# Kernel optimization log

Hardware: AMD Instinct MI355X
Metric: run time of the kernel (lower is better)

Reference implementation:

```python
import jax, jax.numpy as jnp
import numpy as np

B, T, F, H, O = 64, 500, 89, 512, 72


def setup_inputs() -> dict:
    key = jax.random.key(0)
    ks = jax.random.split(key, 16)
    d = {
        "batch": jax.random.normal(ks[0], (B, T, F), dtype=jnp.float32),
        "lengths": jax.random.randint(ks[1], (B,), 250, T + 1),
    }
    in_sizes = [F, 2 * H, 2 * H]  # layer 0 takes features, layers 1-2 take bidir output
    for i, fi in enumerate(in_sizes):
        d[f"w{i}"] = jax.random.normal(ks[2 + 3 * i], (2 * H, fi), dtype=jnp.float32) / np.sqrt(fi).astype(np.float32)
        d[f"b{i}"] = jnp.zeros((2 * H,), jnp.float32)
        d[f"u{i}"] = jax.random.normal(ks[3 + 3 * i], (2 * H, H), dtype=jnp.float32) / np.sqrt(H).astype(np.float32)
    d["wfc"] = jax.random.normal(ks[12], (O, 2 * H), dtype=jnp.float32) / np.sqrt(2 * H).astype(np.float32)
    d["bfc"] = jnp.zeros((O,), jnp.float32)
    return d


def _ligru_bidir(x, W, b, U):
    # SpeechBrain LiGRU layer: fwd and bwd directions share weights; the
    # time-flipped copy is stacked along the batch dim and one scan is run.
    Bx = x.shape[0]
    xb = jnp.concatenate([x, x[:, ::-1]], axis=0)            # [2B, T, in]
    gates_x = jnp.einsum('btf,gf->tbg', xb, W) + b           # [T, 2B, 2H] precomputed input gates
    h0 = jnp.zeros((2 * Bx, H), x.dtype)

    def step(h, g):
        g = g + h @ U.T                                       # [2B, 2H]
        at, zt = jnp.split(g, 2, axis=-1)
        zt = jax.nn.sigmoid(zt)
        h = zt * h + (1.0 - zt) * jnp.tanh(at)                # nonlinearity='tanh'
        return h, h

    _, hs = jax.lax.scan(step, h0, gates_x)                   # [T, 2B, H]
    hs = jnp.swapaxes(hs, 0, 1)                               # [2B, T, H]
    return jnp.concatenate([hs[:Bx], hs[Bx:, ::-1]], axis=2)  # [B, T, 2H]


def reference(batch, lengths, w0, b0, u0, w1, b1, u1, w2, b2, u2, wfc, bfc):
    x = batch
    for W, b, U in ((w0, b0, u0), (w1, b1, u1), (w2, b2, u2)):
        x = _ligru_bidir(x, W, b, U)
    out = jnp.einsum('bth,oh->bto', x, wfc) + bfc             # [B, T, O]
    # Pack valid frames per utterance: predictions[p:p+len_i] = out[i, :len_i]
    mask = (jnp.arange(T)[None, :] < lengths[:, None]).ravel()  # [B*T]
    order = jnp.argsort(jnp.logical_not(mask), stable=True)     # valid rows first, in order
    total = int(np.asarray(lengths).sum())
    return out.reshape(B * T, O)[order][:total]
```

## Files before the change

kernel.cpp:

```cpp
#include <hip/hip_runtime.h>

typedef _Float16 f16;
typedef _Float16 half8 __attribute__((ext_vector_type(8)));
typedef float f32x4 __attribute__((ext_vector_type(4)));
typedef unsigned int u32;
typedef u32 u32x2 __attribute__((ext_vector_type(2)));
typedef u32 u32x4 __attribute__((ext_vector_type(4)));

__device__ inline float frcp(float x) {
#if __has_builtin(__builtin_amdgcn_rcpf)
  return __builtin_amdgcn_rcpf(x);
#else
  return 1.0f / x;
#endif
}
__device__ inline float fexp2(float x) {
#if __has_builtin(__builtin_amdgcn_exp2f)
  return __builtin_amdgcn_exp2f(x);
#else
  return exp2f(x);
#endif
}


__global__ void k_cvt(const float* __restrict__ s, f16* __restrict__ d, int n) {
  int i = blockIdx.x * 256 + threadIdx.x;
  if (i < n) d[i] = (f16)s[i];
}

__global__ void k_zero(u32* __restrict__ p, int n) {
  int i = blockIdx.x * 256 + threadIdx.x;
  if (i < n) p[i] = 0u;
}

__global__ void k_w0pad(const float* __restrict__ w0, f16* __restrict__ d) {
  int i = blockIdx.x * 256 + threadIdx.x;
  if (i >= 1024 * 96) return;
  int row = i / 96, c = i % 96;
  d[i] = (c < 89) ? (f16)w0[row * 89 + c] : (f16)0.f;
}

__global__ void k_xb0(const float* __restrict__ x, f16* __restrict__ d) {
  int i = blockIdx.x * 256 + threadIdx.x;
  if (i >= 128 * 500 * 96) return;
  int f = i % 96;
  int t = (i / 96) % 500;
  int s = i / (96 * 500);
  float v = 0.f;
  if (f < 89) {
    if (s < 64) v = x[((size_t)s * 500 + t) * 89 + f];
    else        v = x[((size_t)(s - 64) * 500 + (499 - t)) * 89 + f];
  }
  d[i] = (f16)v;
}

__global__ void k_offs(const int* __restrict__ lens, int* __restrict__ offs) {
  if (threadIdx.x == 0 && blockIdx.x == 0) {
    int s = 0;
    for (int i = 0; i < 64; ++i) { offs[i] = s; s += lens[i]; }
  }
}

template <int MODE>
__global__ __launch_bounds__(256) void k_gates(const f16* __restrict__ Aw,
                                               const f16* __restrict__ W16,
                                               const float* __restrict__ bias,
                                               f16* __restrict__ gates) {
  constexpr int KW = MODE ? 1024 : 96;
  const int t = blockIdx.x;
  const int nb = blockIdx.y * 128;
  const int tid = threadIdx.x;
  const int w = tid >> 6, l = tid & 63, c = l & 15, rg = l >> 4;
  const int wr = w >> 1, wc = w & 1;

  __shared__ f16 As[128 * 32];
  __shared__ f16 Bs[128 * 32];

  f32x4 acc[4][4] = {};

  const int srow = tid >> 1;
  const int seg = (tid & 1) * 16;
  const int ch0 = seg >> 3;
  const int wsw = (srow >> 1) & 3;

  for (int kb = 0; kb < KW; kb += 32) {
    const f16* pa;
    if (MODE == 0) {
      pa = Aw + ((size_t)srow * 500 + t) * 96 + kb + seg;
    } else {
      int f0 = kb + seg;
      int half = f0 >> 9;
      int col = f0 & 511;
      int s = srow;
      int seq, time;
      if (s < 64) { seq = half ? 64 + s : s;  time = half ? 499 - t : t; }
      else        { seq = half ? s : s - 64;  time = half ? t : 499 - t; }
      pa = Aw + ((size_t)seq * 500 + time) * 512 + col;
    }
    const f16* pb = W16 + (size_t)(nb + srow) * KW + kb + seg;
    half8 a0 = *(const half8*)pa;
    half8 a1 = *(const half8*)(pa + 8);
    half8 b0 = *(const half8*)pb;
    half8 b1 = *(const half8*)(pb + 8);
    __syncthreads();
    *(half8*)&As[srow * 32 + ((ch0 + 0) ^ wsw) * 8] = a0;
    *(half8*)&As[srow * 32 + ((ch0 + 1) ^ wsw) * 8] = a1;
    *(half8*)&Bs[srow * 32 + ((ch0 + 0) ^ wsw) * 8] = b0;
    *(half8*)&Bs[srow * 32 + ((ch0 + 1) ^ wsw) * 8] = b1;
    __syncthreads();
    half8 aF[4], bF[4];
#pragma unroll
    for (int i = 0; i < 4; ++i) {
      int row = wr * 64 + i * 16 + c;
      aF[i] = *(const half8*)&As[row * 32 + ((rg ^ ((row >> 1) & 3)) * 8)];
    }
#pragma unroll
    for (int j = 0; j < 4; ++j) {
      int row = wc * 64 + j * 16 + c;
      bF[j] = *(const half8*)&Bs[row * 32 + ((rg ^ ((row >> 1) & 3)) * 8)];
    }
#pragma unroll
    for (int i = 0; i < 4; ++i)
#pragma unroll
      for (int j = 0; j < 4; ++j)
        acc[i][j] = __builtin_amdgcn_mfma_f32_16x16x32_f16(aF[i], bF[j], acc[i][j], 0, 0, 0);
  }

#pragma unroll
  for (int j = 0; j < 4; ++j) {
    int n = nb + wc * 64 + j * 16 + c;
    float bj = bias[n];
#pragma unroll
    for (int i = 0; i < 4; ++i) {
#pragma unroll
      for (int r = 0; r < 4; ++r) {
        int m = wr * 64 + i * 16 + rg * 4 + r;
        gates[((size_t)t * 128 + m) * 1024 + n] = (f16)(acc[i][j][r] + bj);
      }
    }
  }
}

__global__ __launch_bounds__(256, 1) void k_rec(const f16* __restrict__ gates,
                                                const f16* __restrict__ U,
                                                f16* __restrict__ hs,
                                                f16* __restrict__ hx,
                                                u32* __restrict__ flags,
                                                int tagbase) {
  const int sg = blockIdx.x & 7, cg = blockIdx.x >> 3;
  const int tid = threadIdx.x;
  const int l = tid & 63, w = tid >> 6, c = l & 15, rg = l >> 4;
  const int s0 = sg * 16;
  const int hcol = cg * 64 + w * 16;
  const int an0 = hcol, zn0 = 512 + hcol;

  __shared__ f16 hlds[8192 + 4 * 256];

  half8 ua[16], uz[16];
#pragma unroll
  for (int kt = 0; kt < 16; ++kt) {
    ua[kt] = *(const half8*)(U + (size_t)(an0 + c) * 512 + kt * 32 + rg * 8);
    uz[kt] = *(const half8*)(U + (size_t)(zn0 + c) * 512 + kt * 32 + rg * 8);
  }

  float hold[4] = {0.f, 0.f, 0.f, 0.f};

  f16 ga[4], gz[4];
  {
    const f16* gb = gates + ((size_t)0 * 128 + s0 + rg * 4) * 1024;
#pragma unroll
    for (int r = 0; r < 4; ++r) { ga[r] = gb[r * 1024 + an0 + c]; gz[r] = gb[r * 1024 + zn0 + c]; }
  }

  const int ktp = cg * 2 + (w >> 1);
  const int pbase = ktp * 512 + (w & 1) * 256;
  f16* scr = &hlds[8192 + w * 256];
  const int scri = (c >> 3) * 128 + (c & 7);
  const int srow2 = (l >> 1) & 15;
  const int col2 = ktp * 32 + ((w & 1) * 2 + (l >> 5)) * 8 + (l & 1) * 4;

  const size_t tileoff = (size_t)sg * 8192;

  for (int t = 0; t < 500; ++t) {
#pragma unroll
    for (int kt = 0; kt < 16; ++kt) asm volatile("" : "+v"(ua[kt]), "+v"(uz[kt]));

    u32x4 d0, d1, d2, d3;
    if (t == 0) {
      d0 = (u32x4){0u, 0u, 0u, 0u}; d1 = d0; d2 = d0; d3 = d0;
    } else {
      const u32 tgt = (u32)(tagbase + t);
      const u32* fl = flags + sg * 32 + (l & 31);
      int guard = 0;
      for (;;) {
        u32 f = __hip_atomic_load(fl, __ATOMIC_RELAXED, __HIP_MEMORY_SCOPE_AGENT);
        if (__all((int)(f >= tgt))) break;
        if (++guard > (1 << 15)) break;
      }
      const f16* src = hx + (size_t)(t & 1) * 65536 + tileoff + (size_t)tid * 32;
      asm volatile("global_load_dwordx4 %0, %1, off sc0 sc1" : "=v"(d0) : "v"(src) : "memory");
      asm volatile("global_load_dwordx4 %0, %1, off sc0 sc1" : "=v"(d1) : "v"(src + 8) : "memory");
      asm volatile("global_load_dwordx4 %0, %1, off sc0 sc1" : "=v"(d2) : "v"(src + 16) : "memory");
      asm volatile("global_load_dwordx4 %0, %1, off sc0 sc1" : "=v"(d3) : "v"(src + 24) : "memory");
      asm volatile("s_waitcnt vmcnt(0)"
                   : "+v"(d0), "+v"(d1), "+v"(d2), "+v"(d3) : : "memory");
    }
    *(u32x4*)&hlds[tid * 32 + 0]  = d0;
    *(u32x4*)&hlds[tid * 32 + 8]  = d1;
    *(u32x4*)&hlds[tid * 32 + 16] = d2;
    *(u32x4*)&hlds[tid * 32 + 24] = d3;
    __syncthreads();

    f32x4 acc_a, acc_z;
#pragma unroll
    for (int r = 0; r < 4; ++r) { acc_a[r] = (float)ga[r]; acc_z[r] = (float)gz[r]; }
#pragma unroll
    for (int kt = 0; kt < 16; ++kt) {
      half8 aF = *(const half8*)&hlds[kt * 512 + l * 8];
      acc_a = __builtin_amdgcn_mfma_f32_16x16x32_f16(aF, ua[kt], acc_a, 0, 0, 0);
      acc_z = __builtin_amdgcn_mfma_f32_16x16x32_f16(aF, uz[kt], acc_z, 0, 0, 0);
    }

#pragma unroll
    for (int r = 0; r < 4; ++r) {
      float av = acc_a[r];
      float zv = acc_z[r];
      float zs = frcp(1.f + fexp2(-1.44269504f * zv));
      float u2 = fexp2(2.88539008f * av);
      float th = 1.f - 2.f * frcp(u2 + 1.f);
      float hn = th + zs * (hold[r] - th);
      hold[r] = hn;
      scr[scri + (rg * 4 + r) * 8] = (f16)hn;
    }
    u32x2 pkt = *(const u32x2*)&scr[l * 4];
    {
      f16* dst = hx + (size_t)((t + 1) & 1) * 65536 + tileoff + pbase + (size_t)l * 4;
      asm volatile("global_store_dwordx2 %0, %1, off sc0 sc1" :: "v"(dst), "v"(pkt) : "memory");
    }
    asm volatile("s_waitcnt vmcnt(0)" ::: "memory");
    if (l == 0)
      __hip_atomic_store(&flags[sg * 32 + cg * 4 + w], (u32)(tagbase + t + 1),
                         __ATOMIC_RELAXED, __HIP_MEMORY_SCOPE_AGENT);

    *(u32x2*)&hs[((size_t)(s0 + srow2) * 500 + t) * 512 + col2] = pkt;

    int tn = (t + 1 < 500) ? t + 1 : 499;
    const f16* gb = gates + ((size_t)tn * 128 + s0 + rg * 4) * 1024;
#pragma unroll
    for (int r = 0; r < 4; ++r) { ga[r] = gb[r * 1024 + an0 + c]; gz[r] = gb[r * 1024 + zn0 + c]; }
  }
}

__global__ __launch_bounds__(256) void k_fc(const f16* __restrict__ hs,
                                            const f16* __restrict__ wfc,
                                            const float* __restrict__ bfc,
                                            const int* __restrict__ lens,
                                            const int* __restrict__ offs,
                                            float* __restrict__ out) {
  const int b = blockIdx.x, chunk = blockIdx.y;
  const int tid = threadIdx.x;
  __shared__ f16 X[16][1032];
#pragma unroll
  for (int ii = 0; ii < 8; ++ii) {
    int sg = ii * 256 + tid;
    int row = sg >> 7;
    int f = (sg & 127) * 8;
    int t = chunk * 16 + row;
    int tt = t < 500 ? t : 499;
    int half = f >> 9, col = f & 511;
    int seq = half ? 64 + b : b;
    int time = half ? 499 - tt : tt;
    *(half8*)&X[row][f] = *(const half8*)&hs[((size_t)seq * 500 + time) * 512 + col];
  }
  __syncthreads();
  int row = tid >> 4, og = tid & 15;
  int t = chunk * 16 + row;
  int len = lens[b];
  float acc[5];
#pragma unroll
  for (int j = 0; j < 5; ++j) {
    int o = j * 16 + og;
    acc[j] = (o < 72) ? bfc[o] : 0.f;
  }
  for (int k8 = 0; k8 < 128; ++k8) {
    half8 x8 = *(const half8*)&X[row][k8 * 8];
    float xf[8];
#pragma unroll
    for (int e = 0; e < 8; ++e) xf[e] = (float)x8[e];
#pragma unroll
    for (int j = 0; j < 5; ++j) {
      int o = j * 16 + og;
      int oc = o < 72 ? o : 0;
      half8 w8 = *(const half8*)&wfc[(size_t)oc * 1024 + k8 * 8];
#pragma unroll
      for (int e = 0; e < 8; ++e) acc[j] += xf[e] * (float)w8[e];
    }
  }
  if (t < 500 && t < len) {
    size_t base = ((size_t)offs[b] + t) * 72;
#pragma unroll
    for (int j = 0; j < 5; ++j) {
      int o = j * 16 + og;
      if (o < 72) out[base + o] = acc[j];
    }
  }
}


extern "C" void kernel_launch(void* const* d_in, const int* in_sizes, int n_in,
                              void* d_out, int out_size, void* d_ws, size_t ws_size,
                              hipStream_t stream) {
  const float* batch = (const float*)d_in[0];
  const int*   lens  = (const int*)d_in[1];
  const float* w0 = (const float*)d_in[2];
  const float* b0 = (const float*)d_in[3];
  const float* u0 = (const float*)d_in[4];
  const float* w1 = (const float*)d_in[5];
  const float* b1 = (const float*)d_in[6];
  const float* u1 = (const float*)d_in[7];
  const float* w2 = (const float*)d_in[8];
  const float* b2 = (const float*)d_in[9];
  const float* u2 = (const float*)d_in[10];
  const float* wfc = (const float*)d_in[11];
  const float* bfc = (const float*)d_in[12];
  float* out = (float*)d_out;

  char* ws = (char*)d_ws;
  const size_t GATES_OFF = 0;
  const size_t HS_OFF    = 131072000;
  const size_t XB0_OFF   = 196608000;
  const size_t W0P_OFF   = 208896000;
  const size_t W1_OFF    = 209092608;
  const size_t W2_OFF    = 211189760;
  const size_t U0_OFF    = 213286912;
  const size_t U1_OFF    = 214335488;
  const size_t U2_OFF    = 215384064;
  const size_t WFC_OFF   = 216432640;
  const size_t OFFS_OFF  = 216580096;
  const size_t HX_OFF    = 216581120;
  const size_t FLAGS_OFF = 216843264;

  f16* g_gates = (f16*)(ws + GATES_OFF);
  f16* g_hs    = (f16*)(ws + HS_OFF);
  f16* g_xb0   = (f16*)(ws + XB0_OFF);
  f16* g_w0p   = (f16*)(ws + W0P_OFF);
  f16* g_w1    = (f16*)(ws + W1_OFF);
  f16* g_w2    = (f16*)(ws + W2_OFF);
  f16* g_u0    = (f16*)(ws + U0_OFF);
  f16* g_u1    = (f16*)(ws + U1_OFF);
  f16* g_u2    = (f16*)(ws + U2_OFF);
  f16* g_wfc   = (f16*)(ws + WFC_OFF);
  int* g_offs  = (int*)(ws + OFFS_OFF);
  f16* g_hx    = (f16*)(ws + HX_OFF);
  u32* g_flags = (u32*)(ws + FLAGS_OFF);

  hipLaunchKernelGGL(k_offs, dim3(1), dim3(64), 0, stream, lens, g_offs);

  auto cvt = [&](const float* s, f16* d, int n) {
    hipLaunchKernelGGL(k_cvt, dim3((n + 255) / 256), dim3(256), 0, stream, s, d, n);
  };
  cvt(w1, g_w1, 1024 * 1024);
  cvt(w2, g_w2, 1024 * 1024);
  cvt(u0, g_u0, 1024 * 512);
  cvt(u1, g_u1, 1024 * 512);
  cvt(u2, g_u2, 1024 * 512);
  cvt(wfc, g_wfc, 72 * 1024);
  hipLaunchKernelGGL(k_w0pad, dim3((1024 * 96 + 255) / 256), dim3(256), 0, stream, w0, g_w0p);
  hipLaunchKernelGGL(k_xb0, dim3((128 * 500 * 96 + 255) / 256), dim3(256), 0, stream, batch, g_xb0);
  hipLaunchKernelGGL(k_zero, dim3(1), dim3(256), 0, stream, g_flags, 256);

  hipLaunchKernelGGL((k_gates<0>), dim3(500, 8), dim3(256), 0, stream, g_xb0, g_w0p, b0, g_gates);
  hipLaunchKernelGGL(k_rec, dim3(64), dim3(256), 0, stream, g_gates, g_u0, g_hs, g_hx, g_flags, 0);
  hipLaunchKernelGGL((k_gates<1>), dim3(500, 8), dim3(256), 0, stream, g_hs, g_w1, b1, g_gates);
  hipLaunchKernelGGL(k_rec, dim3(64), dim3(256), 0, stream, g_gates, g_u1, g_hs, g_hx, g_flags, 512);
  hipLaunchKernelGGL((k_gates<1>), dim3(500, 8), dim3(256), 0, stream, g_hs, g_w2, b2, g_gates);
  hipLaunchKernelGGL(k_rec, dim3(64), dim3(256), 0, stream, g_gates, g_u2, g_hs, g_hx, g_flags, 1024);

  hipLaunchKernelGGL(k_fc, dim3(64, 32), dim3(256), 0, stream, g_hs, g_wfc, bfc, lens, g_offs, out);
}
```

Baseline: 4.898 ms.

## Stage recurrent weights in LDS and prefetch fragment-ordered gates four steps ahead

Measured after the change: 6.323 ms. 29.1% more time.

```diff
diff --git a/kernel.cpp b/kernel.cpp
--- a/kernel.cpp
+++ b/kernel.cpp
@@ -126,16 +126,23 @@
         acc[i][j] = __builtin_amdgcn_mfma_f32_16x16x32_f16(aF[i], bF[j], acc[i][j], 0, 0, 0);
   }
 
+  const int tq = t >> 2, ts = t & 3;
 #pragma unroll
   for (int j = 0; j < 4; ++j) {
     int n = nb + wc * 64 + j * 16 + c;
     float bj = bias[n];
+    int az = n >> 9, nn = n & 511;
+    int cg2 = nn >> 6, w2 = (nn >> 4) & 3, c2 = nn & 15;
 #pragma unroll
     for (int i = 0; i < 4; ++i) {
 #pragma unroll
       for (int r = 0; r < 4; ++r) {
         int m = wr * 64 + i * 16 + rg * 4 + r;
-        gates[((size_t)t * 128 + m) * 1024 + n] = (f16)(acc[i][j][r] + bj);
+        int sg2 = m >> 4, sr = m & 15;
+        int l2 = (sr >> 2) * 16 + c2;
+        size_t off = (size_t)tq * 524288 + (size_t)sg2 * 65536 + (size_t)cg2 * 8192 +
+                     (size_t)w2 * 2048 + (size_t)l2 * 32 + ts * 8 + az * 4 + (sr & 3);
+        gates[off] = (f16)(acc[i][j][r] + bj);
       }
     }
   }
@@ -147,107 +154,128 @@
                                                 f16* __restrict__ hx,
                                                 u32* __restrict__ flags,
                                                 int tagbase) {
-  const int sg = blockIdx.x & 7, cg = blockIdx.x >> 3;
+  extern __shared__ f16 smem[];
+  f16* ulds = smem;
+  f16* hlds = smem + 65536;
+  f16* scrb = smem + 65536 + 8192;
+
+  const int bid = blockIdx.x;
+  const int sg = bid & 7, cg = bid >> 3;
   const int tid = threadIdx.x;
   const int l = tid & 63, w = tid >> 6, c = l & 15, rg = l >> 4;
   const int s0 = sg * 16;
-  const int hcol = cg * 64 + w * 16;
-  const int an0 = hcol, zn0 = 512 + hcol;
-
-  __shared__ f16 hlds[8192 + 4 * 256];
-
-  half8 ua[16], uz[16];
-#pragma unroll
-  for (int kt = 0; kt < 16; ++kt) {
-    ua[kt] = *(const half8*)(U + (size_t)(an0 + c) * 512 + kt * 32 + rg * 8);
-    uz[kt] = *(const half8*)(U + (size_t)(zn0 + c) * 512 + kt * 32 + rg * 8);
-  }
-
-  float hold[4] = {0.f, 0.f, 0.f, 0.f};
-
-  f16 ga[4], gz[4];
+
   {
-    const f16* gb = gates + ((size_t)0 * 128 + s0 + rg * 4) * 1024;
-#pragma unroll
-    for (int r = 0; r < 4; ++r) { ga[r] = gb[r * 1024 + an0 + c]; gz[r] = gb[r * 1024 + zn0 + c]; }
-  }
+    const f16* Ua = U + (size_t)cg * 64 * 512;
+    const f16* Uz = U + (size_t)(512 + cg * 64) * 512;
+#pragma unroll
+    for (int it = 0; it < 16; ++it) {
+      int rr = (it & 3) * 16 + c;
+      int chunk = (it >> 2) * 16 + w * 4 + rg;
+      int col = chunk * 8;
+      half8 va = *(const half8*)(Ua + (size_t)rr * 512 + col);
+      half8 vz = *(const half8*)(Uz + (size_t)rr * 512 + col);
+      int wv = rr >> 4, cc = rr & 15, kt = col >> 5, rg2 = (col >> 3) & 3;
+      int base = (wv * 32 + kt) * 512 + (rg2 * 16 + cc) * 8;
+      *(half8*)&ulds[base] = va;
+      *(half8*)&ulds[base + 8192] = vz;
+    }
+  }
+  __syncthreads();
 
   const int ktp = cg * 2 + (w >> 1);
   const int pbase = ktp * 512 + (w & 1) * 256;
-  f16* scr = &hlds[8192 + w * 256];
-  const int scri = (c >> 3) * 128 + (c & 7);
+  f16* scr = scrb + w * 384;
   const int srow2 = (l >> 1) & 15;
   const int col2 = ktp * 32 + ((w & 1) * 2 + (l >> 5)) * 8 + (l & 1) * 4;
-
   const size_t tileoff = (size_t)sg * 8192;
-
-  for (int t = 0; t < 500; ++t) {
-#pragma unroll
-    for (int kt = 0; kt < 16; ++kt) asm volatile("" : "+v"(ua[kt]), "+v"(uz[kt]));
-
-    u32x4 d0, d1, d2, d3;
-    if (t == 0) {
-      d0 = (u32x4){0u, 0u, 0u, 0u}; d1 = d0; d2 = d0; d3 = d0;
-    } else {
-      const u32 tgt = (u32)(tagbase + t);
-      const u32* fl = flags + sg * 32 + (l & 31);
-      int guard = 0;
-      for (;;) {
-        u32 f = __hip_atomic_load(fl, __ATOMIC_RELAXED, __HIP_MEMORY_SCOPE_AGENT);
-        if (__all((int)(f >= tgt))) break;
-        if (++guard > (1 << 15)) break;
+  const u32* flbase = flags + sg * 32;
+  u32* myflag = flags + sg * 32 + cg * 4 + w;
+
+  const f16* gbase = gates + (size_t)sg * 65536 + (size_t)cg * 8192 +
+                     (size_t)w * 2048 + (size_t)l * 32;
+  u32x4 gcur[4], gnxt[4];
+#pragma unroll
+  for (int q = 0; q < 4; ++q) gcur[q] = *(const u32x4*)(gbase + q * 8);
+
+  float hold[4] = {0.f, 0.f, 0.f, 0.f};
+
+  for (int tb = 0; tb < 125; ++tb) {
+#pragma unroll
+    for (int ts = 0; ts < 4; ++ts) {
+      const int t = tb * 4 + ts;
+      u32x4 d0, d1, d2, d3;
+      if (t == 0) {
+        d0 = (u32x4){0u, 0u, 0u, 0u}; d1 = d0; d2 = d0; d3 = d0;
+      } else {
+        const u32 tgt = (u32)(tagbase + t);
+        const u32* fl = flbase + (l & 31);
+        int g2 = 0;
+        for (;;) {
+          u32 f = __hip_atomic_load(fl, __ATOMIC_RELAXED, __HIP_MEMORY_SCOPE_AGENT);
+          if (__all((int)(f >= tgt))) break;
+          if (++g2 > (1 << 15)) break;
+        }
+        const f16* src = hx + (size_t)(t & 1) * 65536 + tileoff + (size_t)tid * 32;
+        asm volatile("global_load_dwordx4 %0, %1, off sc0 sc1" : "=v"(d0) : "v"(src) : "memory");
+        asm volatile("global_load_dwordx4 %0, %1, off sc0 sc1" : "=v"(d1) : "v"(src + 8) : "memory");
+        asm volatile("global_load_dwordx4 %0, %1, off sc0 sc1" : "=v"(d2) : "v"(src + 16) : "memory");
+        asm volatile("global_load_dwordx4 %0, %1, off sc0 sc1" : "=v"(d3) : "v"(src + 24) : "memory");
+        asm volatile("s_waitcnt vmcnt(0)"
+                     : "+v"(d0), "+v"(d1), "+v"(d2), "+v"(d3) : : "memory");
       }
-      const f16* src = hx + (size_t)(t & 1) * 65536 + tileoff + (size_t)tid * 32;
-      asm volatile("global_load_dwordx4 %0, %1, off sc0 sc1" : "=v"(d0) : "v"(src) : "memory");
-      asm volatile("global_load_dwordx4 %0, %1, off sc0 sc1" : "=v"(d1) : "v"(src + 8) : "memory");
-      asm volatile("global_load_dwordx4 %0, %1, off sc0 sc1" : "=v"(d2) : "v"(src + 16) : "memory");
-      asm volatile("global_load_dwordx4 %0, %1, off sc0 sc1" : "=v"(d3) : "v"(src + 24) : "memory");
-      asm volatile("s_waitcnt vmcnt(0)"
-                   : "+v"(d0), "+v"(d1), "+v"(d2), "+v"(d3) : : "memory");
-    }
-    *(u32x4*)&hlds[tid * 32 + 0]  = d0;
-    *(u32x4*)&hlds[tid * 32 + 8]  = d1;
-    *(u32x4*)&hlds[tid * 32 + 16] = d2;
-    *(u32x4*)&hlds[tid * 32 + 24] = d3;
-    __syncthreads();
-
-    f32x4 acc_a, acc_z;
-#pragma unroll
-    for (int r = 0; r < 4; ++r) { acc_a[r] = (float)ga[r]; acc_z[r] = (float)gz[r]; }
-#pragma unroll
-    for (int kt = 0; kt < 16; ++kt) {
-      half8 aF = *(const half8*)&hlds[kt * 512 + l * 8];
-      acc_a = __builtin_amdgcn_mfma_f32_16x16x32_f16(aF, ua[kt], acc_a, 0, 0, 0);
-      acc_z = __builtin_amdgcn_mfma_f32_16x16x32_f16(aF, uz[kt], acc_z, 0, 0, 0);
-    }
-
-#pragma unroll
-    for (int r = 0; r < 4; ++r) {
-      float av = acc_a[r];
-      float zv = acc_z[r];
-      float zs = frcp(1.f + fexp2(-1.44269504f * zv));
-      float u2 = fexp2(2.88539008f * av);
-      float th = 1.f - 2.f * frcp(u2 + 1.f);
-      float hn = th + zs * (hold[r] - th);
-      hold[r] = hn;
-      scr[scri + (rg * 4 + r) * 8] = (f16)hn;
-    }
-    u32x2 pkt = *(const u32x2*)&scr[l * 4];
-    {
+
+      if (ts == 0) {
+        int tqn = (tb < 124) ? tb + 1 : 124;
+        const f16* gb2 = gbase + (size_t)tqn * 524288;
+#pragma unroll
+        for (int q = 0; q < 4; ++q) gnxt[q] = *(const u32x4*)(gb2 + q * 8);
+      }
+
+      *(u32x4*)&hlds[tid * 32 + 0]  = d0;
+      *(u32x4*)&hlds[tid * 32 + 8]  = d1;
+      *(u32x4*)&hlds[tid * 32 + 16] = d2;
+      *(u32x4*)&hlds[tid * 32 + 24] = d3;
+      __syncthreads();
+
+      f32x4 acc_a, acc_z;
+      const half8 gv = __builtin_bit_cast(half8, gcur[ts]);
+#pragma unroll
+      for (int r = 0; r < 4; ++r) { acc_a[r] = (float)gv[r]; acc_z[r] = (float)gv[4 + r]; }
+#pragma unroll
+      for (int kt = 0; kt < 16; ++kt) {
+        half8 aF = *(const half8*)&hlds[kt * 512 + l * 8];
+        half8 bA = *(const half8*)&ulds[(w * 32 + kt) * 512 + l * 8];
+        half8 bZ = *(const half8*)&ulds[(w * 32 + 16 + kt) * 512 + l * 8];
+        acc_a = __builtin_amdgcn_mfma_f32_16x16x32_f16(aF, bA, acc_a, 0, 0, 0);
+        acc_z = __builtin_amdgcn_mfma_f32_16x16x32_f16(aF, bZ, acc_z, 0, 0, 0);
+      }
+      __syncthreads();
+
+#pragma unroll
+      for (int r = 0; r < 4; ++r) {
+        float av = acc_a[r];
+        float zv = acc_z[r];
+        float zs = frcp(1.f + fexp2(-1.44269504f * zv));
+        float u2 = fexp2(2.88539008f * av);
+        float th = 1.f - 2.f * frcp(u2 + 1.f);
+        float hn = th + zs * (hold[r] - th);
+        hold[r] = hn;
+        scr[(rg * 4 + r) * 20 + c] = (f16)hn;
+      }
+      u32x2 pkt = *(const u32x2*)&scr[srow2 * 20 + (l >> 5) * 8 + (l & 1) * 4];
+
       f16* dst = hx + (size_t)((t + 1) & 1) * 65536 + tileoff + pbase + (size_t)l * 4;
+      const u32 tg2 = (u32)(tagbase + t + 1);
       asm volatile("global_store_dwordx2 %0, %1, off sc0 sc1" :: "v"(dst), "v"(pkt) : "memory");
-    }
-    asm volatile("s_waitcnt vmcnt(0)" ::: "memory");
-    if (l == 0)
-      __hip_atomic_store(&flags[sg * 32 + cg * 4 + w], (u32)(tagbase + t + 1),
-                         __ATOMIC_RELAXED, __HIP_MEMORY_SCOPE_AGENT);
-
-    *(u32x2*)&hs[((size_t)(s0 + srow2) * 500 + t) * 512 + col2] = pkt;
-
-    int tn = (t + 1 < 500) ? t + 1 : 499;
-    const f16* gb = gates + ((size_t)tn * 128 + s0 + rg * 4) * 1024;
-#pragma unroll
-    for (int r = 0; r < 4; ++r) { ga[r] = gb[r * 1024 + an0 + c]; gz[r] = gb[r * 1024 + zn0 + c]; }
+      asm volatile("s_waitcnt vmcnt(0)" ::: "memory");
+      if (l == 0)
+        __hip_atomic_store(myflag, tg2, __ATOMIC_RELAXED, __HIP_MEMORY_SCOPE_AGENT);
+
+      *(u32x2*)&hs[((size_t)(s0 + srow2) * 500 + t) * 512 + col2] = pkt;
+    }
+#pragma unroll
+    for (int q = 0; q < 4; ++q) gcur[q] = gnxt[q];
   }
 }
 
@@ -354,6 +382,9 @@
   f16* g_hx    = (f16*)(ws + HX_OFF);
   u32* g_flags = (u32*)(ws + FLAGS_OFF);
 
+  const int REC_LDS = (65536 + 8192 + 1536) * 2;
+  hipFuncSetAttribute((const void*)k_rec, hipFuncAttributeMaxDynamicSharedMemorySize, REC_LDS);
+
   hipLaunchKernelGGL(k_offs, dim3(1), dim3(64), 0, stream, lens, g_offs);
 
   auto cvt = [&](const float* s, f16* d, int n) {
@@ -370,11 +401,14 @@
   hipLaunchKernelGGL(k_zero, dim3(1), dim3(256), 0, stream, g_flags, 256);
 
   hipLaunchKernelGGL((k_gates<0>), dim3(500, 8), dim3(256), 0, stream, g_xb0, g_w0p, b0, g_gates);
-  hipLaunchKernelGGL(k_rec, dim3(64), dim3(256), 0, stream, g_gates, g_u0, g_hs, g_hx, g_flags, 0);
+  hipLaunchKernelGGL(k_rec, dim3(64), dim3(256), REC_LDS, stream,
+                     g_gates, g_u0, g_hs, g_hx, g_flags, 0);
   hipLaunchKernelGGL((k_gates<1>), dim3(500, 8), dim3(256), 0, stream, g_hs, g_w1, b1, g_gates);
-  hipLaunchKernelGGL(k_rec, dim3(64), dim3(256), 0, stream, g_gates, g_u1, g_hs, g_hx, g_flags, 512);
+  hipLaunchKernelGGL(k_rec, dim3(64), dim3(256), REC_LDS, stream,
+                     g_gates, g_u1, g_hs, g_hx, g_flags, 512);
   hipLaunchKernelGGL((k_gates<1>), dim3(500, 8), dim3(256), 0, stream, g_hs, g_w2, b2, g_gates);
-  hipLaunchKernelGGL(k_rec, dim3(64), dim3(256), 0, stream, g_gates, g_u2, g_hs, g_hx, g_flags, 1024);
+  hipLaunchKernelGGL(k_rec, dim3(64), dim3(256), REC_LDS, stream,
+                     g_gates, g_u2, g_hs, g_hx, g_flags, 1024);
 
   hipLaunchKernelGGL(k_fc, dim3(64, 32), dim3(256), 0, stream, g_hs, g_wfc, bfc, lens, g_offs, out);
 }
```
